# Kernel tuning notes

Measured on AMD Instinct MI355X. Metric: run time of the kernel, lower is better.

Reference implementation:

```python
import jax, jax.numpy as jnp
import numpy as np

NUM_HEADS = 16
DIM = 1024

def setup_inputs() -> dict:
    key = jax.random.key(0)
    ks = jax.random.split(key, 12)
    B, N, T, C = 4, 4096, 77, DIM
    s = 1.0 / np.sqrt(C)
    return {
        "hidden_states": jax.random.normal(ks[0], (B, N, C), jnp.float32),
        "encoder_hidden_states": jax.random.normal(ks[1], (B, T, C), jnp.float32),
        "attention_mask": jnp.zeros((B, N, T), jnp.float32),
        "Wq": jax.random.normal(ks[2], (C, C), jnp.float32) * s,
        "bq": jnp.zeros((C,), jnp.float32),
        "Wk": jax.random.normal(ks[3], (C, C), jnp.float32) * s,
        "bk": jnp.zeros((C,), jnp.float32),
        "Wv": jax.random.normal(ks[4], (C, C), jnp.float32) * s,
        "bv": jnp.zeros((C,), jnp.float32),
        "Wo": jax.random.normal(ks[5], (C, C), jnp.float32) * s,
        "bo": jnp.zeros((C,), jnp.float32),
    }

def reference(hidden_states, encoder_hidden_states, attention_mask,
              Wq, bq, Wk, bk, Wv, bv, Wo, bo):
    B, N, C = hidden_states.shape
    T = encoder_hidden_states.shape[1]
    H = NUM_HEADS
    D = C // H
    # QKV projections (torch Linear: x @ W.T + b)
    q = (hidden_states @ Wq.T + bq).reshape(B, N, H, D).transpose(0, 2, 1, 3)   # bhnd
    k = (encoder_hidden_states @ Wk.T + bk).reshape(B, T, H, D).transpose(0, 2, 1, 3)  # bhtd
    v = (encoder_hidden_states @ Wv.T + bv).reshape(B, T, H, D).transpose(0, 2, 1, 3)  # bhtd
    scale = 1.0 / jnp.sqrt(jnp.asarray(D, q.dtype))
    # scores [B,H,N,T]; additive mask broadcast over heads
    scores = jnp.einsum('bhnd,bhtd->bhnt', q, k) * scale + attention_mask[:, None, :, :]
    attn = jax.nn.softmax(scores, axis=-1)
    out = jnp.einsum('bhnt,bhtd->bhnd', attn, v)
    out = out.transpose(0, 2, 1, 3).reshape(B, N, C)
    return out @ Wo.T + bo
```

## Files before the change

kernel.cpp:

```cpp
#include <hip/hip_runtime.h>
#include <cstdint>

typedef __bf16 bf16x8 __attribute__((ext_vector_type(8)));
typedef float f32x4 __attribute__((ext_vector_type(4)));
typedef unsigned short u16;
typedef unsigned int u32;

__device__ __forceinline__ u16 f2bf(float f) {
    u32 u = __builtin_bit_cast(u32, f);
    u += 0x7fffu + ((u >> 16) & 1u);
    return (u16)(u >> 16);
}

__device__ __forceinline__ void gl_lds16(const u16* g, u16* l) {
    __builtin_amdgcn_global_load_lds(
        (const __attribute__((address_space(1))) void*)g,
        (__attribute__((address_space(3))) void*)l,
        16, 0, 0);
}

__device__ __forceinline__ f32x4 mfma16(bf16x8 a, bf16x8 b, f32x4 c) {
    return __builtin_amdgcn_mfma_f32_16x16x32_bf16(a, b, c, 0, 0, 0);
}


struct CvtAll {
    const float* s[6];
    u16* d[6];
    int srcn[6];
    int totn[6];
    int off[6];
};

__global__ void cvt_all(CvtAll a) {
    const int blk = blockIdx.x;
    int seg = 0;
#pragma unroll
    for (int s = 1; s < 6; ++s) seg += (blk >= a.off[s]);
    const int i = ((blk - a.off[seg]) * 256 + threadIdx.x) * 4;
    if (i >= a.totn[seg]) return;
    float4 v = make_float4(0.f, 0.f, 0.f, 0.f);
    if (i < a.srcn[seg]) v = *(const float4*)&a.s[seg][i];
    ushort4 o;
    o.x = f2bf(v.x); o.y = f2bf(v.y); o.z = f2bf(v.z); o.w = f2bf(v.w);
    *(ushort4*)&a.d[seg][i] = o;
}

__device__ __forceinline__ void store_out(u16* C, long idx, float v) { C[idx] = f2bf(v); }
__device__ __forceinline__ void store_out(float* C, long idx, float v) { C[idx] = v; }

template <typename OutT, bool BA, bool BC>
__global__ __launch_bounds__(512, 2) void gemmP(
    const u16* __restrict__ A, const u16* __restrict__ W,
    const float* __restrict__ bias, OutT* __restrict__ C,
    int M, int N, int K) {
    __shared__ __align__(16) u16 As[2][256 * 32];
    __shared__ __align__(16) u16 Bs[2][128 * 32];

    const int tid = threadIdx.x;
    const int wid = tid >> 6, l = tid & 63;
    const int wr = wid >> 1, wc = wid & 1;
    const int l15 = l & 15, lg = l >> 4;

    const int lin = blockIdx.y * gridDim.x + blockIdx.x;
    const int cpx = (gridDim.x * gridDim.y) >> 3;
    const int swz = (lin & 7) * cpx + (lin >> 3);
    const long tn = swz & 7;
    const long tm = swz >> 3;

    const int srp = tid >> 3;
    const int sv = (tid & 7) ^ (srp & 7);
    const int sE = (sv >> 2) & 1;
    const int sKC = sv & 3;
    const long ar0 = tm * 256 + 2 * srp + sE;
    const long brow = tn * 128 + 2 * srp + sE;
    const long aRB = ar0 >> 2;
    const int aSub = (int)(ar0 & 3) * 16 + (sKC & 1) * 8;
    const int aCB = sKC >> 1;

    const int NT = K >> 5;

#define STAGE(bufi, t_)                                                        \
    do {                                                                       \
        if (BA) {                                                              \
            const long cb_ = (long)((t_) * 2 + aCB) * (M >> 2);                \
            gl_lds16(A + (cb_ + aRB) * 64 + aSub, &As[bufi][tid * 8]);         \
            gl_lds16(A + (cb_ + aRB + 32) * 64 + aSub,                         \
                     &As[bufi][4096 + tid * 8]);                               \
        } else {                                                               \
            gl_lds16(A + ar0 * (long)K + (t_) * 32 + sKC * 8,                  \
                     &As[bufi][tid * 8]);                                      \
            gl_lds16(A + (ar0 + 128) * (long)K + (t_) * 32 + sKC * 8,          \
                     &As[bufi][4096 + tid * 8]);                               \
        }                                                                      \
        gl_lds16(W + brow * (long)K + (t_) * 32 + sKC * 8,                     \
                 &Bs[bufi][tid * 8]);                                          \
    } while (0)

    const int e = l15 & 1;
    const int rphA = wr * 32 + (l15 >> 1);
    const int rphB = wc * 32 + (l15 >> 1);
    const int pA = ((e * 4 + lg) ^ (rphA & 7)) * 8;
    const int pB = ((e * 4 + lg) ^ (rphB & 7)) * 8;
    const int aOff = rphA * 64 + pA;
    const int bOff = rphB * 64 + pB;

    f32x4 acc[4][4] = {};

    STAGE(0, 0);
    __syncthreads();

    for (int t = 0; t < NT; ++t) {
        const int c = t & 1;
        if (t + 1 < NT) STAGE(c ^ 1, t + 1);

        bf16x8 a[4], b[4];
#pragma unroll
        for (int nf = 0; nf < 4; ++nf)
            b[nf] = *(const bf16x8*)&Bs[c][bOff + nf * 512];
#pragma unroll
        for (int mf = 0; mf < 4; ++mf)
            a[mf] = *(const bf16x8*)&As[c][aOff + mf * 512];

        __builtin_amdgcn_s_setprio(1);
#pragma unroll
        for (int mf = 0; mf < 4; ++mf)
#pragma unroll
            for (int nf = 0; nf < 4; ++nf)
                acc[mf][nf] = mfma16(a[mf], b[nf], acc[mf][nf]);
        __builtin_amdgcn_s_setprio(0);
        __syncthreads();
    }
#undef STAGE

    const long row0 = tm * 256 + wr * 64;
    const long col0 = tn * 128 + wc * 64;
    float bv[4];
#pragma unroll
    for (int nf = 0; nf < 4; ++nf) bv[nf] = bias[col0 + nf * 16 + l15];
    if (BC) {
        const long ct0 = col0 >> 4;
        const long rb = row0 >> 2;
#pragma unroll
        for (int mf = 0; mf < 4; ++mf)
#pragma unroll
            for (int nf = 0; nf < 4; ++nf)
#pragma unroll
                for (int r = 0; r < 4; ++r) {
                    const long idx =
                        ((ct0 + nf) * (long)(M >> 2) + rb + mf * 4 + lg) * 64 +
                        r * 16 + l15;
                    store_out(C, idx, acc[mf][nf][r] + bv[nf]);
                }
    } else {
#pragma unroll
        for (int mf = 0; mf < 4; ++mf)
#pragma unroll
            for (int nf = 0; nf < 4; ++nf)
#pragma unroll
                for (int r = 0; r < 4; ++r) {
                    const long row = row0 + mf * 16 + lg * 4 + r;
                    const long col = col0 + nf * 16 + l15;
                    store_out(C, row * N + col, acc[mf][nf][r] + bv[nf]);
                }
    }
}

template <bool VT>
__device__ __forceinline__ void gemm128_body(
    const u16* __restrict__ A, const u16* __restrict__ W,
    const float* __restrict__ bias, u16* __restrict__ C,
    int N, int K) {
    __shared__ u16 As[128 * 64];
    __shared__ u16 Bs[128 * 64];
    const int tid = threadIdx.x;
    const int w = tid >> 6, l = tid & 63;
    const int wr = w >> 1, wc = w & 1;
    const int l15 = l & 15, lg = l >> 4;
    const long tm = blockIdx.y, tn = blockIdx.x;
    const u16* Ab = A + tm * 128 * (long)K;
    const u16* Bb = W + tn * 128 * (long)K;

    f32x4 acc[4][4] = {};

    for (int k0 = 0; k0 < K; k0 += 64) {
#pragma unroll
        for (int t = 0; t < 4; ++t) {
            int i = t * 256 + tid;
            int row = i >> 3, cc = i & 7;
            gl_lds16(Ab + (long)row * K + k0 + cc * 8, &As[i * 8]);
            gl_lds16(Bb + (long)row * K + k0 + cc * 8, &Bs[i * 8]);
        }
        __syncthreads();
#pragma unroll
        for (int kk = 0; kk < 64; kk += 32) {
            bf16x8 a[4], b[4];
#pragma unroll
            for (int m = 0; m < 4; ++m)
                a[m] = *(const bf16x8*)&As[(wr * 64 + m * 16 + l15) * 64 + kk + lg * 8];
#pragma unroll
            for (int n = 0; n < 4; ++n)
                b[n] = *(const bf16x8*)&Bs[(wc * 64 + n * 16 + l15) * 64 + kk + lg * 8];
#pragma unroll
            for (int m = 0; m < 4; ++m)
#pragma unroll
                for (int n = 0; n < 4; ++n)
                    acc[m][n] = mfma16(a[m], b[n], acc[m][n]);
        }
        __syncthreads();
    }

    const long row0 = tm * 128 + wr * 64;
    const long col0 = tn * 128 + wc * 64;
#pragma unroll
    for (int m = 0; m < 4; ++m)
#pragma unroll
        for (int n = 0; n < 4; ++n)
#pragma unroll
            for (int r = 0; r < 4; ++r) {
                const float v = acc[m][n][r] + bias[col0 + n * 16 + l15];
                if (VT) {
                    const int row = (int)(row0 + m * 16 + lg * 4 + r);
                    if (row < 308) {
                        const int bb = row / 77;
                        const int t = row - bb * 77;
                        const int ch = (int)(col0 + n * 16 + l15);
                        const long idx = (long)bb * 98304 +
                                         ((long)(t >> 4) * 256 + (ch >> 2)) * 64 +
                                         (ch & 3) * 16 + (t & 15);
                        C[idx] = f2bf(v);
                    }
                } else {
                    const long idx = (((col0 >> 4) + n) * 96L + (row0 >> 2) + m * 4 + lg) * 64 +
                                     r * 16 + l15;
                    C[idx] = f2bf(v);
                }
            }
}

__global__ __launch_bounds__(256) void gemm_kv(
    const u16* __restrict__ A,
    const u16* __restrict__ Wk, const float* __restrict__ bk, u16* __restrict__ Ko,
    const u16* __restrict__ Wv, const float* __restrict__ bv, u16* __restrict__ Vo,
    int N, int K) {
    if (blockIdx.z == 0)
        gemm128_body<false>(A, Wk, bk, Ko, N, K);
    else
        gemm128_body<true>(A, Wv, bv, Vo, N, K);
}

__global__ __launch_bounds__(256, 4) void attn_fused(
    const u16* __restrict__ Q,
    const u16* __restrict__ Kb,
    const u16* __restrict__ Vt,
    const float* __restrict__ mask,
    u16* __restrict__ Ao) {
    __shared__ u16 Ps[128 * 104];

    const int h = blockIdx.x, b = blockIdx.y, nt = blockIdx.z;
    const int tid = threadIdx.x;
    const int w = tid >> 6, l = tid & 63;
    const int l15 = l & 15, lg = l >> 4;

    const int qrow = b * 4096 + nt * 128 + w * 32;

    f32x4 acc[5][2] = {};
#pragma unroll
    for (int kk = 0; kk < 64; kk += 32) {
        const int d = kk + lg * 8;
        const int cb = h * 4 + (d >> 4);
        const int dlow = d & 15;
        bf16x8 kf[5], qf[2];
#pragma unroll
        for (int n = 0; n < 5; ++n) {
            const int row = b * 77 + n * 16 + l15;
            kf[n] = *(const bf16x8*)&Kb[((long)cb * 96 + (row >> 2)) * 64 +
                                        (row & 3) * 16 + dlow];
        }
#pragma unroll
        for (int m = 0; m < 2; ++m) {
            const int row = qrow + m * 16 + l15;
            qf[m] = *(const bf16x8*)&Q[((long)cb * 4096 + (row >> 2)) * 64 +
                                       (row & 3) * 16 + dlow];
        }
#pragma unroll
        for (int n = 0; n < 5; ++n)
#pragma unroll
            for (int m = 0; m < 2; ++m)
                acc[n][m] = mfma16(kf[n], qf[m], acc[n][m]);
    }

    const float* mrow0 = mask + ((long)b * 4096 + nt * 128 + w * 32) * 77;
#pragma unroll
    for (int m = 0; m < 2; ++m) {
        const float* mrow = mrow0 + (m * 16 + l15) * 77;
        float vals[5][4];
        float rmax = -3e38f;
#pragma unroll
        for (int n = 0; n < 5; ++n) {
            const int t0 = n * 16 + lg * 4;
#pragma unroll
            for (int r = 0; r < 4; ++r) {
                float mv;
                if (n < 4)
                    mv = mrow[t0 + r];
                else
                    mv = (t0 + r < 77) ? mrow[t0 + r] : -1e30f;
                const float v = acc[n][m][r] * 0.125f + mv;
                vals[n][r] = v;
                rmax = fmaxf(rmax, v);
            }
        }
        rmax = fmaxf(rmax, __shfl_xor(rmax, 16, 64));
        rmax = fmaxf(rmax, __shfl_xor(rmax, 32, 64));
        float s = 0.f;
#pragma unroll
        for (int n = 0; n < 5; ++n)
#pragma unroll
            for (int r = 0; r < 4; ++r) {
                const float e = __expf(vals[n][r] - rmax);
                vals[n][r] = e;
                s += e;
            }
        s += __shfl_xor(s, 16, 64);
        s += __shfl_xor(s, 32, 64);
        const float inv = 1.f / s;
#pragma unroll
        for (int n = 0; n < 5; ++n) {
            const u32 lo = (u32)f2bf(vals[n][0] * inv) |
                           ((u32)f2bf(vals[n][1] * inv) << 16);
            const u32 hi = (u32)f2bf(vals[n][2] * inv) |
                           ((u32)f2bf(vals[n][3] * inv) << 16);
            *(uint2*)&Ps[(w * 32 + m * 16 + l15) * 104 + n * 16 + lg * 4] =
                make_uint2(lo, hi);
        }
        *(uint2*)&Ps[(w * 32 + m * 16 + l15) * 104 + 80 + lg * 4] = make_uint2(0, 0);
    }

    f32x4 o[2][4] = {};
#pragma unroll
    for (int kt = 0; kt < 96; kt += 32) {
        bf16x8 pa[2], vf[4];
#pragma unroll
        for (int m = 0; m < 2; ++m)
            pa[m] = *(const bf16x8*)&Ps[(w * 32 + m * 16 + l15) * 104 + kt + lg * 8];
        const int t0 = kt + lg * 8;
#pragma unroll
        for (int n = 0; n < 4; ++n) {
            const int ch = h * 64 + n * 16 + l15;
            vf[n] = *(const bf16x8*)&Vt[(long)b * 98304 +
                                        ((long)(t0 >> 4) * 256 + (ch >> 2)) * 64 +
                                        (ch & 3) * 16 + (t0 & 15)];
        }
#pragma unroll
        for (int m = 0; m < 2; ++m)
#pragma unroll
            for (int n = 0; n < 4; ++n)
                o[m][n] = mfma16(pa[m], vf[n], o[m][n]);
    }

#pragma unroll
    for (int m = 0; m < 2; ++m)
#pragma unroll
        for (int n = 0; n < 4; ++n)
#pragma unroll
            for (int r = 0; r < 4; ++r) {
                const long idx = ((long)(h * 4 + n) * 4096 +
                                  b * 1024 + nt * 32 + w * 8 + m * 4 + lg) * 64 +
                                 r * 16 + l15;
                Ao[idx] = f2bf(o[m][n][r]);
            }
}

extern "C" void kernel_launch(void* const* d_in, const int* in_sizes, int n_in,
                              void* d_out, int out_size, void* d_ws, size_t ws_size,
                              hipStream_t stream) {
    const float* hidden = (const float*)d_in[0];
    const float* enc = (const float*)d_in[1];
    const float* mask = (const float*)d_in[2];
    const float* Wq = (const float*)d_in[3];
    const float* bq = (const float*)d_in[4];
    const float* Wk = (const float*)d_in[5];
    const float* bk = (const float*)d_in[6];
    const float* Wv = (const float*)d_in[7];
    const float* bv = (const float*)d_in[8];
    const float* Wo = (const float*)d_in[9];
    const float* bo = (const float*)d_in[10];
    float* out = (float*)d_out;

    char* ws = (char*)d_ws;
    u16* hiddenB = (u16*)(ws);
    u16* Qb = (u16*)(ws + 33554432L);
    u16* AoB = (u16*)(ws + 2 * 33554432L);
    u16* WqB = (u16*)(ws + 3 * 33554432L);
    u16* WkB = WqB + 1048576;
    u16* WvB = WkB + 1048576;
    u16* WoB = WvB + 1048576;
    u16* encB = WoB + 1048576;
    u16* Kbuf = encB + 393216;
    u16* VtBuf = Kbuf + 393216;

    CvtAll ca;
    ca.s[0] = hidden; ca.d[0] = hiddenB; ca.srcn[0] = 16777216; ca.totn[0] = 16777216;
    ca.s[1] = Wq;  ca.d[1] = WqB; ca.srcn[1] = 1048576; ca.totn[1] = 1048576;
    ca.s[2] = Wk;  ca.d[2] = WkB; ca.srcn[2] = 1048576; ca.totn[2] = 1048576;
    ca.s[3] = Wv;  ca.d[3] = WvB; ca.srcn[3] = 1048576; ca.totn[3] = 1048576;
    ca.s[4] = Wo;  ca.d[4] = WoB; ca.srcn[4] = 1048576; ca.totn[4] = 1048576;
    ca.s[5] = enc; ca.d[5] = encB; ca.srcn[5] = 315392; ca.totn[5] = 393216;
    ca.off[0] = 0;
    ca.off[1] = 16384;
    ca.off[2] = 17408;
    ca.off[3] = 18432;
    ca.off[4] = 19456;
    ca.off[5] = 20480;
    cvt_all<<<dim3(20864), 256, 0, stream>>>(ca);

    gemmP<u16, false, true><<<dim3(8, 64), 512, 0, stream>>>(
        hiddenB, WqB, bq, Qb, 16384, 1024, 1024);
    gemm_kv<<<dim3(8, 3, 2), 256, 0, stream>>>(encB, WkB, bk, Kbuf, WvB, bv, VtBuf, 1024, 1024);

    attn_fused<<<dim3(16, 4, 32), 256, 0, stream>>>(Qb, Kbuf, VtBuf, mask, AoB);

    gemmP<float, true, false><<<dim3(8, 64), 512, 0, stream>>>(
        AoB, WoB, bo, out, 16384, 1024, 1024);
}
```

Before: 161.9 us.

## Fuse fp32-to-bf16 conversion of hidden states into Q projection GEMM loads

Removes the separate conversion pass over the 64MB fp32 hidden_states tensor. The Q-projection GEMM now loads fp32 rows directly through registers, converts them to bf16 and writes them into LDS after the MFMA block, overlapping the load with compute. This saves a full write and re-read of a 32MB bf16 buffer. In exchange, the GEMM reads twice as many A bytes, and register-staged loads replace the asynchronous global-to-LDS path, which raises register pressure and conversion ALU work inside the main loop.

After: 191.5 us. 18.3% more time.

```diff
diff --git a/kernel.cpp b/kernel.cpp
--- a/kernel.cpp
+++ b/kernel.cpp
@@ -25,18 +25,18 @@
 
 
 struct CvtAll {
-    const float* s[6];
-    u16* d[6];
-    int srcn[6];
-    int totn[6];
-    int off[6];
+    const float* s[5];
+    u16* d[5];
+    int srcn[5];
+    int totn[5];
+    int off[5];
 };
 
 __global__ void cvt_all(CvtAll a) {
     const int blk = blockIdx.x;
     int seg = 0;
 #pragma unroll
-    for (int s = 1; s < 6; ++s) seg += (blk >= a.off[s]);
+    for (int s = 1; s < 5; ++s) seg += (blk >= a.off[s]);
     const int i = ((blk - a.off[seg]) * 256 + threadIdx.x) * 4;
     if (i >= a.totn[seg]) return;
     float4 v = make_float4(0.f, 0.f, 0.f, 0.f);
@@ -49,13 +49,15 @@
 __device__ __forceinline__ void store_out(u16* C, long idx, float v) { C[idx] = f2bf(v); }
 __device__ __forceinline__ void store_out(float* C, long idx, float v) { C[idx] = v; }
 
-template <typename OutT, bool BA, bool BC>
+template <typename OutT, int AM, bool BC>
 __global__ __launch_bounds__(512, 2) void gemmP(
-    const u16* __restrict__ A, const u16* __restrict__ W,
+    const void* __restrict__ Av, const u16* __restrict__ W,
     const float* __restrict__ bias, OutT* __restrict__ C,
     int M, int N, int K) {
     __shared__ __align__(16) u16 As[2][256 * 32];
     __shared__ __align__(16) u16 Bs[2][128 * 32];
+    const u16* Amt = (const u16*)Av;
+    const float* Af = (const float*)Av;
 
     const int tid = threadIdx.x;
     const int wid = tid >> 6, l = tid & 63;
@@ -80,21 +82,37 @@
 
     const int NT = K >> 5;
 
-#define STAGE(bufi, t_)                                                        \
-    do {                                                                       \
-        if (BA) {                                                              \
-            const long cb_ = (long)((t_) * 2 + aCB) * (M >> 2);                \
-            gl_lds16(A + (cb_ + aRB) * 64 + aSub, &As[bufi][tid * 8]);         \
-            gl_lds16(A + (cb_ + aRB + 32) * 64 + aSub,                         \
-                     &As[bufi][4096 + tid * 8]);                               \
-        } else {                                                               \
-            gl_lds16(A + ar0 * (long)K + (t_) * 32 + sKC * 8,                  \
-                     &As[bufi][tid * 8]);                                      \
-            gl_lds16(A + (ar0 + 128) * (long)K + (t_) * 32 + sKC * 8,          \
-                     &As[bufi][4096 + tid * 8]);                               \
-        }                                                                      \
-        gl_lds16(W + brow * (long)K + (t_) * 32 + sKC * 8,                     \
-                 &Bs[bufi][tid * 8]);                                          \
+#define STAGE_B(bufi, t_)                                                     \
+    gl_lds16(W + brow * (long)K + (t_) * 32 + sKC * 8, &Bs[bufi][tid * 8])
+#define STAGE_AMT(bufi, t_)                                                   \
+    do {                                                                      \
+        const long cb_ = (long)((t_) * 2 + aCB) * (M >> 2);                   \
+        gl_lds16(Amt + (cb_ + aRB) * 64 + aSub, &As[bufi][tid * 8]);          \
+        gl_lds16(Amt + (cb_ + aRB + 32) * 64 + aSub,                          \
+                 &As[bufi][4096 + tid * 8]);                                  \
+    } while (0)
+#define LOAD_AF(t_)                                                           \
+    do {                                                                      \
+        const float* p0_ = Af + ar0 * (long)K + (t_) * 32 + sKC * 8;          \
+        fa0 = *(const float4*)p0_;                                            \
+        fa1 = *(const float4*)(p0_ + 4);                                      \
+        const float* p1_ = Af + (ar0 + 128) * (long)K + (t_) * 32 + sKC * 8;  \
+        fa2 = *(const float4*)p1_;                                            \
+        fa3 = *(const float4*)(p1_ + 4);                                      \
+    } while (0)
+#define WRITE_AF(bufi)                                                        \
+    do {                                                                      \
+        uint4 w0_, w1_;                                                       \
+        w0_.x = (u32)f2bf(fa0.x) | ((u32)f2bf(fa0.y) << 16);                  \
+        w0_.y = (u32)f2bf(fa0.z) | ((u32)f2bf(fa0.w) << 16);                  \
+        w0_.z = (u32)f2bf(fa1.x) | ((u32)f2bf(fa1.y) << 16);                  \
+        w0_.w = (u32)f2bf(fa1.z) | ((u32)f2bf(fa1.w) << 16);                  \
+        w1_.x = (u32)f2bf(fa2.x) | ((u32)f2bf(fa2.y) << 16);                  \
+        w1_.y = (u32)f2bf(fa2.z) | ((u32)f2bf(fa2.w) << 16);                  \
+        w1_.z = (u32)f2bf(fa3.x) | ((u32)f2bf(fa3.y) << 16);                  \
+        w1_.w = (u32)f2bf(fa3.z) | ((u32)f2bf(fa3.w) << 16);                  \
+        *(uint4*)&As[bufi][tid * 8] = w0_;                                    \
+        *(uint4*)&As[bufi][4096 + tid * 8] = w1_;                             \
     } while (0)
 
     const int e = l15 & 1;
@@ -106,13 +124,25 @@
     const int bOff = rphB * 64 + pB;
 
     f32x4 acc[4][4] = {};
-
-    STAGE(0, 0);
+    float4 fa0, fa1, fa2, fa3;
+
+    if (AM == 2) {
+        LOAD_AF(0);
+        STAGE_B(0, 0);
+        WRITE_AF(0);
+    } else {
+        STAGE_AMT(0, 0);
+        STAGE_B(0, 0);
+    }
     __syncthreads();
 
     for (int t = 0; t < NT; ++t) {
         const int c = t & 1;
-        if (t + 1 < NT) STAGE(c ^ 1, t + 1);
+        if (t + 1 < NT) {
+            if (AM == 2) LOAD_AF(t + 1);
+            else STAGE_AMT(c ^ 1, t + 1);
+            STAGE_B(c ^ 1, t + 1);
+        }
 
         bf16x8 a[4], b[4];
 #pragma unroll
@@ -129,9 +159,14 @@
             for (int nf = 0; nf < 4; ++nf)
                 acc[mf][nf] = mfma16(a[mf], b[nf], acc[mf][nf]);
         __builtin_amdgcn_s_setprio(0);
+
+        if (AM == 2 && t + 1 < NT) WRITE_AF(c ^ 1);
         __syncthreads();
     }
-#undef STAGE
+#undef STAGE_B
+#undef STAGE_AMT
+#undef LOAD_AF
+#undef WRITE_AF
 
     const long row0 = tm * 256 + wr * 64;
     const long col0 = tn * 128 + wc * 64;
@@ -389,7 +424,6 @@
     float* out = (float*)d_out;
 
     char* ws = (char*)d_ws;
-    u16* hiddenB = (u16*)(ws);
     u16* Qb = (u16*)(ws + 33554432L);
     u16* AoB = (u16*)(ws + 2 * 33554432L);
     u16* WqB = (u16*)(ws + 3 * 33554432L);
@@ -401,26 +435,24 @@
     u16* VtBuf = Kbuf + 393216;
 
     CvtAll ca;
-    ca.s[0] = hidden; ca.d[0] = hiddenB; ca.srcn[0] = 16777216; ca.totn[0] = 16777216;
-    ca.s[1] = Wq;  ca.d[1] = WqB; ca.srcn[1] = 1048576; ca.totn[1] = 1048576;
-    ca.s[2] = Wk;  ca.d[2] = WkB; ca.srcn[2] = 1048576; ca.totn[2] = 1048576;
-    ca.s[3] = Wv;  ca.d[3] = WvB; ca.srcn[3] = 1048576; ca.totn[3] = 1048576;
-    ca.s[4] = Wo;  ca.d[4] = WoB; ca.srcn[4] = 1048576; ca.totn[4] = 1048576;
-    ca.s[5] = enc; ca.d[5] = encB; ca.srcn[5] = 315392; ca.totn[5] = 393216;
+    ca.s[0] = Wq;  ca.d[0] = WqB; ca.srcn[0] = 1048576; ca.totn[0] = 1048576;
+    ca.s[1] = Wk;  ca.d[1] = WkB; ca.srcn[1] = 1048576; ca.totn[1] = 1048576;
+    ca.s[2] = Wv;  ca.d[2] = WvB; ca.srcn[2] = 1048576; ca.totn[2] = 1048576;
+    ca.s[3] = Wo;  ca.d[3] = WoB; ca.srcn[3] = 1048576; ca.totn[3] = 1048576;
+    ca.s[4] = enc; ca.d[4] = encB; ca.srcn[4] = 315392; ca.totn[4] = 393216;
     ca.off[0] = 0;
-    ca.off[1] = 16384;
-    ca.off[2] = 17408;
-    ca.off[3] = 18432;
-    ca.off[4] = 19456;
-    ca.off[5] = 20480;
-    cvt_all<<<dim3(20864), 256, 0, stream>>>(ca);
-
-    gemmP<u16, false, true><<<dim3(8, 64), 512, 0, stream>>>(
-        hiddenB, WqB, bq, Qb, 16384, 1024, 1024);
+    ca.off[1] = 1024;
+    ca.off[2] = 2048;
+    ca.off[3] = 3072;
+    ca.off[4] = 4096;
+    cvt_all<<<dim3(4480), 256, 0, stream>>>(ca);
+
+    gemmP<u16, 2, true><<<dim3(8, 64), 512, 0, stream>>>(
+        hidden, WqB, bq, Qb, 16384, 1024, 1024);
     gemm_kv<<<dim3(8, 3, 2), 256, 0, stream>>>(encB, WkB, bk, Kbuf, WvB, bv, VtBuf, 1024, 1024);
 
     attn_fused<<<dim3(16, 4, 32), 256, 0, stream>>>(Qb, Kbuf, VtBuf, mask, AoB);
 
-    gemmP<float, true, false><<<dim3(8, 64), 512, 0, stream>>>(
+    gemmP<float, 1, false><<<dim3(8, 64), 512, 0, stream>>>(
         AoB, WoB, bo, out, 16384, 1024, 1024);
 }
```
